# Kernel tuning notes

Hardware: AMD Instinct MI355X
Metric: run time of the kernel (lower is better)

Reference implementation:

```python
import jax, jax.numpy as jnp
import numpy as np

HID = 1024
BATCH = 32
SRC = 2048

def setup_inputs() -> dict:
    key = jax.random.key(0)
    k1, k2, k3, k4, k5 = jax.random.split(key, 5)
    hidden = jax.random.normal(k1, (BATCH, HID), dtype=jnp.float32)
    encoder_outputs = jax.random.normal(k2, (BATCH, SRC, HID), dtype=jnp.float32)
    # nn.Linear(2H, H): weight [H, 2H], bias [H]
    lim = 1.0 / np.sqrt(2 * HID)
    attn_w = jax.random.uniform(k3, (HID, 2 * HID), dtype=jnp.float32, minval=-lim, maxval=lim)
    attn_b = jax.random.uniform(k4, (HID,), dtype=jnp.float32, minval=-lim, maxval=lim)
    v = jax.random.uniform(k5, (HID,), dtype=jnp.float32)  # torch.rand
    return {"hidden": hidden, "encoder_outputs": encoder_outputs,
            "attn_w": attn_w, "attn_b": attn_b, "v": v}

def reference(hidden, encoder_outputs, attn_w, attn_b, v):
    # Split the concat linear: cat([hidden, enc]) @ W^T == hidden @ Wh^T + enc @ We^T
    w_h = attn_w[:, :HID]          # [H, H] acts on repeated hidden
    w_e = attn_w[:, HID:]          # [H, H] acts on encoder outputs
    # energy: [B, S, H]
    energy = jnp.tanh(
        jnp.einsum('bh,oh->bo', hidden, w_h)[:, None, :]
        + jnp.einsum('bsh,oh->bso', encoder_outputs, w_e)
        + attn_b
    )
    scores = jnp.einsum('bso,o->bs', energy, v)  # [B, S]
    return jax.nn.softmax(scores, axis=1)
```

## Files before the change

kernel.cpp:

```cpp
#include <hip/hip_runtime.h>
#include <hip/hip_bf16.h>

#define HID    1024
#define NBATCH 32
#define SRC    2048
#define MROWS  (NBATCH * SRC)
#define BM     256
#define BN     256
#define BK     64
#define NTILES (HID / BK)

typedef _Float16 f16;
typedef f16   f16x8 __attribute__((ext_vector_type(8)));
typedef f16   f16x4 __attribute__((ext_vector_type(4)));
typedef float f32x4 __attribute__((ext_vector_type(4)));

#define BAR()   asm volatile("s_barrier" ::: "memory")
#define LGKM0() asm volatile("s_waitcnt lgkmcnt(0)" ::: "memory")

__device__ __forceinline__ float fast_tanh(float x) {
  x = fminf(fmaxf(x, -15.f), 15.f);
  float e = __expf(2.f * x);
  return (e - 1.f) / (e + 1.f);
}

__device__ __forceinline__ f16* LAp(char* lds, int c, int row, int col) {
  return (f16*)(lds + c * 65536 + row * 128 + ((col ^ ((row & 7) << 3)) << 1));
}
__device__ __forceinline__ f16* LBp(char* lds, int c, int row, int col) {
  return (f16*)(lds + c * 65536 + 32768 + row * 128 + ((col ^ ((row & 7) << 3)) << 1));
}

__global__ void convw_k(const float* __restrict__ attn_w, f16* __restrict__ Wf) {
  int idx = blockIdx.x * 256 + threadIdx.x;
  int j = idx * 4;
  int o = j >> 10, h = j & 1023;
  f32x4 d = *(const f32x4*)(attn_w + (size_t)o * 2048 + HID + h);
  f16x4 q = { (f16)d[0], (f16)d[1], (f16)d[2], (f16)d[3] };
  *(f16x4*)(Wf + (size_t)o * HID + h) = q;
}

__global__ void hvec_k(const float* __restrict__ hidden,
                       const float* __restrict__ attn_w,
                       const float* __restrict__ attn_b,
                       float* __restrict__ hvec) {
  int idx = blockIdx.x * 256 + threadIdx.x;
  int b = idx >> 10, o = idx & 1023;
  const float* wrow = attn_w + (size_t)o * 2048;
  const float* hrow = hidden + (size_t)b * HID;
  float acc = 0.f;
  for (int h = 0; h < HID; h += 4) {
    f32x4 wv = *(const f32x4*)(wrow + h);
    f32x4 hv = *(const f32x4*)(hrow + h);
    acc += wv[0]*hv[0] + wv[1]*hv[1] + wv[2]*hv[2] + wv[3]*hv[3];
  }
  hvec[idx] = acc + attn_b[o];
}


#define CVT8(lo, hi) (f16x8){ (f16)(lo)[0], (f16)(lo)[1], (f16)(lo)[2], (f16)(lo)[3], \
                              (f16)(hi)[0], (f16)(hi)[1], (f16)(hi)[2], (f16)(hi)[3] }

#define ISSUE_A1(t) { const float* p_ = Ab + (size_t)srow * HID + (t) * BK + scolh; \
  sa0 = *(const f32x4*)p_; sa1 = *(const f32x4*)(p_ + 4); \
  sa2 = *(const f32x4*)(p_ + 8); sa3 = *(const f32x4*)(p_ + 12); }
#define ISSUE_A2(t) { const float* p_ = Ab + (size_t)srow * HID + (t) * BK + scolh + 16; \
  sa4 = *(const f32x4*)p_; sa5 = *(const f32x4*)(p_ + 4); \
  sa6 = *(const f32x4*)(p_ + 8); sa7 = *(const f32x4*)(p_ + 12); }
#define ISSUE_B(t)  { const f16* p_ = Bb + (size_t)srow * HID + (t) * BK + scolh; \
  sb0 = *(const f16x8*)p_; sb1 = *(const f16x8*)(p_ + 8); \
  sb2 = *(const f16x8*)(p_ + 16); sb3 = *(const f16x8*)(p_ + 24); }
#define WRITE_A1(cc) { *(f16x8*)LAp(lds, cc, srow, scolh)      = CVT8(sa0, sa1); \
                       *(f16x8*)LAp(lds, cc, srow, scolh + 8)  = CVT8(sa2, sa3); }
#define WRITE_A2(cc) { *(f16x8*)LAp(lds, cc, srow, scolh + 16) = CVT8(sa4, sa5); \
                       *(f16x8*)LAp(lds, cc, srow, scolh + 24) = CVT8(sa6, sa7); }
#define WRITE_B(cc)  { *(f16x8*)LBp(lds, cc, srow, scolh)      = sb0; \
                       *(f16x8*)LBp(lds, cc, srow, scolh + 8)  = sb1; \
                       *(f16x8*)LBp(lds, cc, srow, scolh + 16) = sb2; \
                       *(f16x8*)LBp(lds, cc, srow, scolh + 24) = sb3; }

#define TILE_BODY(cC, tn, DOSTAGE) { \
  const int cn_ = (cC) ^ 1; \
  f16x8 bF[4][2]; \
  _Pragma("unroll") for (int n = 0; n < 4; ++n) \
  _Pragma("unroll") for (int ks = 0; ks < 2; ++ks) \
    bF[n][ks] = *(const f16x8*)LBp(lds, (cC), wc * 64 + n * 16 + lr, ks * 32 + lg * 8); \
  _Pragma("unroll") for (int p = 0; p < 4; ++p) { \
    f16x8 aF[2][2]; \
    _Pragma("unroll") for (int i = 0; i < 2; ++i) \
    _Pragma("unroll") for (int ks = 0; ks < 2; ++ks) \
      aF[i][ks] = *(const f16x8*)LAp(lds, (cC), wr * 128 + (p * 2 + i) * 16 + lr, ks * 32 + lg * 8); \
    if (DOSTAGE) { \
      if (p == 0) { ISSUE_A1(tn); } \
      if (p == 1) { ISSUE_A2(tn); ISSUE_B(tn); } \
      if (p == 2) { WRITE_A1(cn_); } \
      if (p == 3) { WRITE_A2(cn_); WRITE_B(cn_); } \
    } \
    __builtin_amdgcn_s_setprio(1); \
    _Pragma("unroll") for (int ks = 0; ks < 2; ++ks) \
    _Pragma("unroll") for (int i = 0; i < 2; ++i) \
    _Pragma("unroll") for (int n = 0; n < 4; ++n) \
      acc[p * 2 + i][n] = __builtin_amdgcn_mfma_f32_16x16x32_f16(aF[i][ks], bF[n][ks], acc[p * 2 + i][n], 0, 0, 0); \
    __builtin_amdgcn_s_setprio(0); \
    if (p == 3) { LGKM0(); } \
    BAR(); \
  } }

__global__ __launch_bounds__(512, 2) void gemm_fused(
    const float* __restrict__ A,
    const f16*  __restrict__ Wf,
    const float* __restrict__ hvec,
    const float* __restrict__ v,
    float* __restrict__ part)
{
  extern __shared__ __align__(16) char lds[];

  int bid = blockIdx.x;
  int wg = (bid & 7) * 128 + (bid >> 3);
  int m_idx = wg >> 2, n_idx = wg & 3;
  long row0 = (long)m_idx * BM;
  int o0 = n_idx * BN;
  int b = (int)(row0 >> 11);

  int tid = threadIdx.x;
  int l = tid & 63, w = tid >> 6;
  int wr = w >> 2, wc = w & 3;
  int lr = l & 15, lg = l >> 4;

  int srow = tid >> 1, scolh = (tid & 1) * 32;

  const float* Ab = A + row0 * HID;
  const f16*   Bb = Wf + (size_t)o0 * HID;

  f32x4 acc[8][4];
#pragma unroll
  for (int m = 0; m < 8; ++m)
#pragma unroll
    for (int n = 0; n < 4; ++n) acc[m][n] = (f32x4){0.f, 0.f, 0.f, 0.f};

  f32x4 sa0, sa1, sa2, sa3, sa4, sa5, sa6, sa7;
  f16x8 sb0, sb1, sb2, sb3;

  ISSUE_A1(0); ISSUE_A2(0); ISSUE_B(0);
  WRITE_A1(0); WRITE_A2(0); WRITE_B(0);
  LGKM0(); BAR();

  for (int T = 0; T < NTILES - 1; ++T) {
    const int c = T & 1;
    TILE_BODY(c, T + 1, 1);
  }
  TILE_BODY((NTILES - 1) & 1, 0, 0);

  float hvv[4], vvv[4];
#pragma unroll
  for (int n = 0; n < 4; ++n) {
    int o = o0 + wc * 64 + n * 16 + lr;
    hvv[n] = hvec[b * HID + o];
    vvv[n] = v[o];
  }
  float* scf = (float*)lds;
  __syncthreads();
#pragma unroll
  for (int m = 0; m < 8; ++m) {
#pragma unroll
    for (int r = 0; r < 4; ++r) {
      float s = 0.f;
#pragma unroll
      for (int n = 0; n < 4; ++n)
        s += fast_tanh(acc[m][n][r] + hvv[n]) * vvv[n];
      s += __shfl_xor(s, 1); s += __shfl_xor(s, 2);
      s += __shfl_xor(s, 4); s += __shfl_xor(s, 8);
      if (lr == 0) scf[wc * 256 + wr * 128 + m * 16 + lg * 4 + r] = s;
    }
  }
  __syncthreads();
  if (tid < 256) {
    float sum = scf[tid] + scf[256 + tid] + scf[512 + tid] + scf[768 + tid];
    part[(size_t)n_idx * MROWS + row0 + tid] = sum;
  }
}

__global__ void softmax_k(const float* __restrict__ part, float* __restrict__ out) {
  int b = blockIdx.x;
  __shared__ float srow[SRC];
  __shared__ float red[8];
  int tid = threadIdx.x;

  float lmax = -1e30f;
  for (int i = tid; i < SRC; i += 256) {
    float s = 0.f;
#pragma unroll
    for (int t = 0; t < 4; ++t)
      s += part[(size_t)t * MROWS + (size_t)b * SRC + i];
    srow[i] = s;
    lmax = fmaxf(lmax, s);
  }
#pragma unroll
  for (int off = 32; off >= 1; off >>= 1)
    lmax = fmaxf(lmax, __shfl_xor(lmax, off));
  if ((tid & 63) == 0) red[tid >> 6] = lmax;
  __syncthreads();
  float bmax = fmaxf(fmaxf(red[0], red[1]), fmaxf(red[2], red[3]));

  float lsum = 0.f;
  for (int i = tid; i < SRC; i += 256) {
    float e = __expf(srow[i] - bmax);
    srow[i] = e;
    lsum += e;
  }
#pragma unroll
  for (int off = 32; off >= 1; off >>= 1)
    lsum += __shfl_xor(lsum, off);
  if ((tid & 63) == 0) red[4 + (tid >> 6)] = lsum;
  __syncthreads();
  float inv = 1.f / (red[4] + red[5] + red[6] + red[7]);
  for (int i = tid; i < SRC; i += 256)
    out[(size_t)b * SRC + i] = srow[i] * inv;
}

extern "C" void kernel_launch(void* const* d_in, const int* in_sizes, int n_in,
                              void* d_out, int out_size, void* d_ws, size_t ws_size,
                              hipStream_t stream) {
  const float* hidden = (const float*)d_in[0];
  const float* enc    = (const float*)d_in[1];
  const float* attn_w = (const float*)d_in[2];
  const float* attn_b = (const float*)d_in[3];
  const float* v      = (const float*)d_in[4];
  float* out = (float*)d_out;

  char* ws = (char*)d_ws;
  f16*   Wf   = (f16*)ws;
  float* hv   = (float*)(ws + (2u << 20));
  float* part = (float*)(ws + (2u << 20) + (512u << 10));

  convw_k<<<1024, 256, 0, stream>>>(attn_w, Wf);
  hvec_k <<<128,  256, 0, stream>>>(hidden, attn_w, attn_b, hv);
  gemm_fused<<<1024, 512, 131072, stream>>>(enc, Wf, hv, v, part);
  softmax_k<<<NBATCH, 256, 0, stream>>>(part, out);
}
```

Baseline: 319.6 us.

## Restructure GEMM pipeline with direct-to-LDS weight loads and deeper A prefetch

Rewrites the main GEMM loop so the f16 weight tile goes straight from global memory into LDS with global_load_lds, skipping the register round-trip. The fp32 encoder tile is prefetched two tiles ahead into registers and converted to f16 one tile ahead. The MFMA sequence is split into four half-tile quadrants with interleaved LDS fragment reads, and explicit vmcnt waits and sched barriers order the stages. This aims to hide global load latency better, at the cost of more registers and tricky swizzle and wait-count correctness.

New measurement: 333.9 us. 1.04x slower.

```diff
diff --git a/kernel.cpp b/kernel.cpp
--- a/kernel.cpp
+++ b/kernel.cpp
@@ -5,30 +5,27 @@
 #define NBATCH 32
 #define SRC    2048
 #define MROWS  (NBATCH * SRC)
-#define BM     256
-#define BN     256
-#define BK     64
-#define NTILES (HID / BK)
 
 typedef _Float16 f16;
 typedef f16   f16x8 __attribute__((ext_vector_type(8)));
 typedef f16   f16x4 __attribute__((ext_vector_type(4)));
 typedef float f32x4 __attribute__((ext_vector_type(4)));
 
-#define BAR()   asm volatile("s_barrier" ::: "memory")
-#define LGKM0() asm volatile("s_waitcnt lgkmcnt(0)" ::: "memory")
+#define BAR()    __builtin_amdgcn_s_barrier()
+#define LGKM0()  asm volatile("s_waitcnt lgkmcnt(0)" ::: "memory")
+#define SCHED0() __builtin_amdgcn_sched_barrier(0)
+#define VMCM(n)  asm volatile("s_waitcnt vmcnt(" #n ")" ::: "memory")
+
+__device__ __forceinline__ void gload_lds16(const void* g, void* l) {
+  __builtin_amdgcn_global_load_lds(
+      (const __attribute__((address_space(1))) void*)g,
+      (__attribute__((address_space(3))) void*)l, 16, 0, 0);
+}
 
 __device__ __forceinline__ float fast_tanh(float x) {
   x = fminf(fmaxf(x, -15.f), 15.f);
   float e = __expf(2.f * x);
   return (e - 1.f) / (e + 1.f);
-}
-
-__device__ __forceinline__ f16* LAp(char* lds, int c, int row, int col) {
-  return (f16*)(lds + c * 65536 + row * 128 + ((col ^ ((row & 7) << 3)) << 1));
-}
-__device__ __forceinline__ f16* LBp(char* lds, int c, int row, int col) {
-  return (f16*)(lds + c * 65536 + 32768 + row * 128 + ((col ^ ((row & 7) << 3)) << 1));
 }
 
 __global__ void convw_k(const float* __restrict__ attn_w, f16* __restrict__ Wf) {
@@ -58,56 +55,63 @@
 }
 
 
-#define CVT8(lo, hi) (f16x8){ (f16)(lo)[0], (f16)(lo)[1], (f16)(lo)[2], (f16)(lo)[3], \
-                              (f16)(hi)[0], (f16)(hi)[1], (f16)(hi)[2], (f16)(hi)[3] }
-
-#define ISSUE_A1(t) { const float* p_ = Ab + (size_t)srow * HID + (t) * BK + scolh; \
-  sa0 = *(const f32x4*)p_; sa1 = *(const f32x4*)(p_ + 4); \
-  sa2 = *(const f32x4*)(p_ + 8); sa3 = *(const f32x4*)(p_ + 12); }
-#define ISSUE_A2(t) { const float* p_ = Ab + (size_t)srow * HID + (t) * BK + scolh + 16; \
-  sa4 = *(const f32x4*)p_; sa5 = *(const f32x4*)(p_ + 4); \
-  sa6 = *(const f32x4*)(p_ + 8); sa7 = *(const f32x4*)(p_ + 12); }
-#define ISSUE_B(t)  { const f16* p_ = Bb + (size_t)srow * HID + (t) * BK + scolh; \
-  sb0 = *(const f16x8*)p_; sb1 = *(const f16x8*)(p_ + 8); \
-  sb2 = *(const f16x8*)(p_ + 16); sb3 = *(const f16x8*)(p_ + 24); }
-#define WRITE_A1(cc) { *(f16x8*)LAp(lds, cc, srow, scolh)      = CVT8(sa0, sa1); \
-                       *(f16x8*)LAp(lds, cc, srow, scolh + 8)  = CVT8(sa2, sa3); }
-#define WRITE_A2(cc) { *(f16x8*)LAp(lds, cc, srow, scolh + 16) = CVT8(sa4, sa5); \
-                       *(f16x8*)LAp(lds, cc, srow, scolh + 24) = CVT8(sa6, sa7); }
-#define WRITE_B(cc)  { *(f16x8*)LBp(lds, cc, srow, scolh)      = sb0; \
-                       *(f16x8*)LBp(lds, cc, srow, scolh + 8)  = sb1; \
-                       *(f16x8*)LBp(lds, cc, srow, scolh + 16) = sb2; \
-                       *(f16x8*)LBp(lds, cc, srow, scolh + 24) = sb3; }
-
-#define TILE_BODY(cC, tn, DOSTAGE) { \
-  const int cn_ = (cC) ^ 1; \
-  f16x8 bF[4][2]; \
-  _Pragma("unroll") for (int n = 0; n < 4; ++n) \
+#define IB4(Tn) do { \
+  _Pragma("unroll") for (int q_ = 0; q_ < 4; ++q_) \
+    gload_lds16(Bb + (size_t)(q_ * 64 + (tid >> 3)) * HID + (Tn) * 64 + scol, \
+                lds + ((Tn) & 1) * 65536 + 32768 + q_ * 8192 + w * 1024); } while (0)
+
+#define IA8(Tn) do { \
+  _Pragma("unroll") for (int q_ = 0; q_ < 4; ++q_) { \
+    const float* p_ = A32 + (size_t)(q_ * 64 + (tid >> 3)) * HID + (Tn) * 64 + scol; \
+    rA[q_ * 2]     = *(const f32x4*)p_; \
+    rA[q_ * 2 + 1] = *(const f32x4*)(p_ + 4); } } while (0)
+
+#define CV8(Tn) do { \
+  _Pragma("unroll") for (int q_ = 0; q_ < 4; ++q_) { \
+    f16x8 h_ = { (f16)rA[q_*2][0], (f16)rA[q_*2][1], (f16)rA[q_*2][2], (f16)rA[q_*2][3], \
+                 (f16)rA[q_*2+1][0], (f16)rA[q_*2+1][1], (f16)rA[q_*2+1][2], (f16)rA[q_*2+1][3] }; \
+    *(f16x8*)(lds + ((Tn) & 1) * 65536 + q_ * 8192 + tid * 16) = h_; } } while (0)
+
+#define RD_A(la_, mh_) do { \
+  _Pragma("unroll") for (int m4 = 0; m4 < 4; ++m4) { \
+    const char* rb = (la_) + (wr * 128 + (mh_) * 64 + m4 * 16 + lr) * 128; \
+    aF[m4][0] = *(const f16x8*)(rb + ((lg ^ sw) << 4)); \
+    aF[m4][1] = *(const f16x8*)(rb + (((4 + lg) ^ sw) << 4)); } } while (0)
+
+#define RD_B(lb_, dst, nh_) do { \
+  _Pragma("unroll") for (int n2 = 0; n2 < 2; ++n2) { \
+    const char* rb = (lb_) + (wc * 64 + (nh_) * 32 + n2 * 16 + lr) * 128; \
+    dst[n2][0] = *(const f16x8*)(rb + ((lg ^ sw) << 4)); \
+    dst[n2][1] = *(const f16x8*)(rb + (((4 + lg) ^ sw) << 4)); } } while (0)
+
+#define MFMA16(bsrc, mh_, nh_) do { \
+  __builtin_amdgcn_s_setprio(1); \
   _Pragma("unroll") for (int ks = 0; ks < 2; ++ks) \
-    bF[n][ks] = *(const f16x8*)LBp(lds, (cC), wc * 64 + n * 16 + lr, ks * 32 + lg * 8); \
-  _Pragma("unroll") for (int p = 0; p < 4; ++p) { \
-    f16x8 aF[2][2]; \
-    _Pragma("unroll") for (int i = 0; i < 2; ++i) \
-    _Pragma("unroll") for (int ks = 0; ks < 2; ++ks) \
-      aF[i][ks] = *(const f16x8*)LAp(lds, (cC), wr * 128 + (p * 2 + i) * 16 + lr, ks * 32 + lg * 8); \
-    if (DOSTAGE) { \
-      if (p == 0) { ISSUE_A1(tn); } \
-      if (p == 1) { ISSUE_A2(tn); ISSUE_B(tn); } \
-      if (p == 2) { WRITE_A1(cn_); } \
-      if (p == 3) { WRITE_A2(cn_); WRITE_B(cn_); } \
-    } \
-    __builtin_amdgcn_s_setprio(1); \
-    _Pragma("unroll") for (int ks = 0; ks < 2; ++ks) \
-    _Pragma("unroll") for (int i = 0; i < 2; ++i) \
-    _Pragma("unroll") for (int n = 0; n < 4; ++n) \
-      acc[p * 2 + i][n] = __builtin_amdgcn_mfma_f32_16x16x32_f16(aF[i][ks], bF[n][ks], acc[p * 2 + i][n], 0, 0, 0); \
-    __builtin_amdgcn_s_setprio(0); \
-    if (p == 3) { LGKM0(); } \
-    BAR(); \
-  } }
-
-__global__ __launch_bounds__(512, 2) void gemm_fused(
-    const float* __restrict__ A,
+  _Pragma("unroll") for (int m4 = 0; m4 < 4; ++m4) \
+  _Pragma("unroll") for (int n2 = 0; n2 < 2; ++n2) \
+    acc[(mh_) * 4 + m4][(nh_) * 2 + n2] = __builtin_amdgcn_mfma_f32_16x16x32_f16( \
+        aF[m4][ks], bsrc[n2][ks], acc[(mh_) * 4 + m4][(nh_) * 2 + n2], 0, 0, 0); \
+  __builtin_amdgcn_s_setprio(0); } while (0)
+
+#define TILE_STD(T_) do { \
+  const char* la_ = lds + ((T_) & 1) * 65536; \
+  const char* lb_ = la_ + 32768; \
+  VMCM(0); SCHED0(); \
+  CV8((T_) + 1); \
+  IB4((T_) + 1); \
+  IA8((T_) + 2); \
+  RD_A(la_, 0); RD_B(lb_, bF0, 0); \
+  MFMA16(bF0, 0, 0); \
+  RD_B(lb_, bF1, 1); \
+  MFMA16(bF1, 0, 1); \
+  RD_A(la_, 1); \
+  MFMA16(bF1, 1, 1); \
+  MFMA16(bF0, 1, 0); \
+  VMCM(8); LGKM0(); SCHED0(); BAR(); \
+} while (0)
+
+__global__ __launch_bounds__(512, 2) void gemm_f16(
+    const float* __restrict__ A32f,
     const f16*  __restrict__ Wf,
     const float* __restrict__ hvec,
     const float* __restrict__ v,
@@ -118,19 +122,19 @@
   int bid = blockIdx.x;
   int wg = (bid & 7) * 128 + (bid >> 3);
   int m_idx = wg >> 2, n_idx = wg & 3;
-  long row0 = (long)m_idx * BM;
-  int o0 = n_idx * BN;
+  long row0 = (long)m_idx * 256;
+  int o0 = n_idx * 256;
   int b = (int)(row0 >> 11);
 
   int tid = threadIdx.x;
   int l = tid & 63, w = tid >> 6;
   int wr = w >> 2, wc = w & 3;
   int lr = l & 15, lg = l >> 4;
-
-  int srow = tid >> 1, scolh = (tid & 1) * 32;
-
-  const float* Ab = A + row0 * HID;
-  const f16*   Bb = Wf + (size_t)o0 * HID;
+  int sw = lr & 7;
+  int scol = ((tid & 7) ^ ((tid >> 3) & 7)) * 8;
+
+  const float* A32 = A32f + row0 * HID;
+  const f16*   Bb  = Wf + (size_t)o0 * HID;
 
   f32x4 acc[8][4];
 #pragma unroll
@@ -138,18 +142,47 @@
 #pragma unroll
     for (int n = 0; n < 4; ++n) acc[m][n] = (f32x4){0.f, 0.f, 0.f, 0.f};
 
-  f32x4 sa0, sa1, sa2, sa3, sa4, sa5, sa6, sa7;
-  f16x8 sb0, sb1, sb2, sb3;
-
-  ISSUE_A1(0); ISSUE_A2(0); ISSUE_B(0);
-  WRITE_A1(0); WRITE_A2(0); WRITE_B(0);
-  LGKM0(); BAR();
-
-  for (int T = 0; T < NTILES - 1; ++T) {
-    const int c = T & 1;
-    TILE_BODY(c, T + 1, 1);
-  }
-  TILE_BODY((NTILES - 1) & 1, 0, 0);
+  f32x4 rA[8];
+  f16x8 aF[4][2], bF0[2][2], bF1[2][2];
+
+  IB4(0);
+  IA8(0);
+  VMCM(0); SCHED0();
+  CV8(0);
+  IA8(1);
+  LGKM0(); SCHED0(); BAR();
+
+#pragma unroll 1
+  for (int E = 0; E < 14; E += 2) {
+    TILE_STD(E);
+    TILE_STD(E + 1);
+  }
+  {
+    const char* la_ = lds;
+    const char* lb_ = la_ + 32768;
+    VMCM(0); SCHED0();
+    CV8(15);
+    IB4(15);
+    RD_A(la_, 0); RD_B(lb_, bF0, 0);
+    MFMA16(bF0, 0, 0);
+    RD_B(lb_, bF1, 1);
+    MFMA16(bF1, 0, 1);
+    RD_A(la_, 1);
+    MFMA16(bF1, 1, 1);
+    MFMA16(bF0, 1, 0);
+    VMCM(0); LGKM0(); SCHED0(); BAR();
+  }
+  {
+    const char* la_ = lds + 65536;
+    const char* lb_ = la_ + 32768;
+    RD_A(la_, 0); RD_B(lb_, bF0, 0);
+    MFMA16(bF0, 0, 0);
+    RD_B(lb_, bF1, 1);
+    MFMA16(bF1, 0, 1);
+    RD_A(la_, 1);
+    MFMA16(bF1, 1, 1);
+    MFMA16(bF0, 1, 0);
+  }
 
   float hvv[4], vvv[4];
 #pragma unroll
@@ -174,13 +207,13 @@
     }
   }
   __syncthreads();
-  if (tid < 256) {
-    float sum = scf[tid] + scf[256 + tid] + scf[512 + tid] + scf[768 + tid];
-    part[(size_t)n_idx * MROWS + row0 + tid] = sum;
-  }
-}
-
-__global__ void softmax_k(const float* __restrict__ part, float* __restrict__ out) {
+  if (tid < 256)
+    part[(size_t)n_idx * MROWS + row0 + tid] =
+        scf[tid] + scf[256 + tid] + scf[512 + tid] + scf[768 + tid];
+}
+
+__global__ void softmax_k(const float* __restrict__ part, float* __restrict__ out,
+                          int nsl) {
   int b = blockIdx.x;
   __shared__ float srow[SRC];
   __shared__ float red[8];
@@ -189,8 +222,7 @@
   float lmax = -1e30f;
   for (int i = tid; i < SRC; i += 256) {
     float s = 0.f;
-#pragma unroll
-    for (int t = 0; t < 4; ++t)
+    for (int t = 0; t < nsl; ++t)
       s += part[(size_t)t * MROWS + (size_t)b * SRC + i];
     srow[i] = s;
     lmax = fmaxf(lmax, s);
@@ -230,11 +262,11 @@
 
   char* ws = (char*)d_ws;
   f16*   Wf   = (f16*)ws;
-  float* hv   = (float*)(ws + (2u << 20));
-  float* part = (float*)(ws + (2u << 20) + (512u << 10));
+  float* hv   = (float*)(ws + (2ull << 20));
+  float* part = (float*)(ws + (2ull << 20) + (128ull << 10));
 
   convw_k<<<1024, 256, 0, stream>>>(attn_w, Wf);
   hvec_k <<<128,  256, 0, stream>>>(hidden, attn_w, attn_b, hv);
-  gemm_fused<<<1024, 512, 131072, stream>>>(enc, Wf, hv, v, part);
-  softmax_k<<<NBATCH, 256, 0, stream>>>(part, out);
-}
+  gemm_f16<<<1024, 512, 131072, stream>>>(enc, Wf, hv, v, part);
+  softmax_k<<<NBATCH, 256, 0, stream>>>(part, out, 4);
+}
```
